# Kernel tuning notes

Hardware: AMD Instinct MI355X
Metric: run time of the kernel (lower is better)

## Reference

```python
import jax, jax.numpy as jnp
import numpy as np

# config (from UnifiedAttentionConfig defaults)
D = 512; H = 8; C = 64; DQ = 256; NI = 2; CI = 64
TOPK = 32; LMAX = 16; NWIN = 128; ROPE_BASE = 10000.0
B = 1; T = 1024; LP = 8; P = T // LP
NEG = -1e30


def _rope_cache(seq_len, dim):
    half = dim // 2
    inv = 1.0 / (ROPE_BASE ** (jnp.arange(half, dtype=jnp.float32) / half))
    f = jnp.arange(seq_len, dtype=jnp.float32)[:, None] * inv[None, :]
    emb = jnp.concatenate([f, f], axis=-1)
    return jnp.cos(emb), jnp.sin(emb)


def _rot(x, cos, sin):
    half = x.shape[-1] // 2
    x1, x2 = x[..., :half], x[..., half:]
    return x * cos + jnp.concatenate([-x2, x1], axis=-1) * sin


def _rms(x, w, eps=1e-6):
    return x * jax.lax.rsqrt(jnp.mean(x * x, axis=-1, keepdims=True) + eps) * w


def _forward(h, W_dq, W_uq, W_csa_kv, W_csa_z, B_csa, W_idx_kv, W_idx_z, B_idx,
             W_iuq, W_w, W_swkv, qnorm_w, knorm_w, W_o, sink_logits,
             phrase_mask, phrase_token_idx, phrase_end_pos):
    Bq, Tq, Dq = h.shape
    Pn, Lmax = phrase_mask.shape[1], phrase_mask.shape[2]
    scale = 1.0 / jnp.sqrt(jnp.float32(C))
    cos, sin = _rope_cache(Tq, C)
    cos_i, sin_i = _rope_cache(Tq, CI)
    # ---- queries: compress -> up-project -> RMSNorm -> RoPE (per-token) ----
    q_lat = h @ W_dq                                      # (B,T,DQ)
    q = (q_lat @ W_uq).reshape(Bq, Tq, H, C)
    q = _rot(_rms(q, qnorm_w), cos[:, None, :], sin[:, None, :])
    # ---- gather phrase tokens ----
    idx = phrase_token_idx.reshape(Bq, Pn * Lmax)
    hp = jnp.take_along_axis(h, idx[:, :, None], axis=1).reshape(Bq, Pn, Lmax, Dq)
    m = phrase_mask                                       # (B,P,Lmax) bool
    # ---- multi-head phrase compression (CSA KV) ----
    c_tok = (hp @ W_csa_kv).reshape(Bq, Pn, Lmax, H, C)
    z = (hp @ W_csa_z).reshape(Bq, Pn, Lmax, H, C) + B_csa[None, None]
    z = jnp.where(m[..., None, None], z, NEG)
    g = jax.nn.softmax(z, axis=2)
    g = jnp.where(m.any(axis=2)[:, :, None, None, None], g, 0.0)
    c_csa = jnp.sum(g * c_tok, axis=2)                    # (B,P,H,C) values
    pos = jnp.clip(phrase_end_pos, 0, Tq - 1)
    k_csa = _rot(_rms(c_csa, knorm_w), cos[pos][:, :, None, :], sin[pos][:, :, None, :])
    # ---- single-head phrase compression (indexer keys) ----
    ck = hp @ W_idx_kv                                    # (B,P,Lmax,CI)
    zk = hp @ W_idx_z + B_idx[None, None]
    zk = jnp.where(m[..., None], zk, NEG)
    gk = jax.nn.softmax(zk, axis=2)
    gk = jnp.where(m.any(axis=2)[:, :, None, None], gk, 0.0)
    k_idx = jnp.sum(gk * ck, axis=2)                      # (B,P,CI)
    k_idx = _rot(k_idx, cos_i[pos], sin_i[pos])
    # ---- lightning indexer + causal top-k routing ----
    q_i = (q_lat @ W_iuq).reshape(Bq, Tq, NI, CI)
    s = jax.nn.relu(jnp.einsum('bthd,bpd->bthp', q_i, k_idx))
    I = jnp.sum(s * (h @ W_w)[..., None], axis=2)         # (B,T,P)
    t_idx = jnp.arange(Tq)
    valid = (phrase_end_pos[:, None, :] <= t_idx[None, :, None]) & (phrase_end_pos[:, None, :] >= 0)
    I = jnp.where(valid, I, NEG)
    vals, sel = jax.lax.top_k(I, TOPK)                    # (B,T,K)
    sel_ok = vals > NEG * 0.5
    k_sel = jnp.take_along_axis(k_csa[:, None], sel[:, :, :, None, None], axis=2)  # (B,T,K,H,C)
    v_sel = jnp.take_along_axis(c_csa[:, None], sel[:, :, :, None, None], axis=2)
    logit_csa = jnp.einsum('bthc,btkhc->bthk', q, k_sel) * scale
    logit_csa = jnp.where(sel_ok[:, :, None, :], logit_csa, NEG)
    # ---- sliding window (fixed mode) ----
    kv = (h @ W_swkv).reshape(Bq, Tq, H, C)
    k_sw = _rot(_rms(kv, knorm_w), cos[:, None, :], sin[:, None, :])
    widx = t_idx[:, None] + jnp.arange(NWIN)[None, :] - (NWIN - 1)  # (T,W)
    w_ok = widx >= 0
    widx_c = jnp.clip(widx, 0, Tq - 1)
    k_win = k_sw[:, widx_c]                               # (B,T,W,H,C)
    v_win = kv[:, widx_c]
    logit_sw = jnp.einsum('bthc,btwhc->bthw', q, k_win) * scale
    logit_sw = jnp.where(w_ok[None, :, None, :], logit_sw, NEG)
    # ---- single softmax over [csa | window | sink] ----
    sink = jnp.broadcast_to(sink_logits.reshape(1, 1, H, 1), (Bq, Tq, H, 1))
    pattn = jax.nn.softmax(jnp.concatenate([logit_csa, logit_sw, sink], axis=-1), axis=-1)
    out = jnp.einsum('bthk,btkhc->bthc', pattn[..., :TOPK], v_sel) \
        + jnp.einsum('bthw,btwhc->bthc', pattn[..., TOPK:TOPK + NWIN], v_win)
    return out.reshape(Bq, Tq, H * C) @ W_o


def setup_inputs() -> dict:
    key = jax.random.key(0)
    ks = jax.random.split(key, 16)
    nrm = lambda k, shp: 0.02 * jax.random.normal(k, shp, dtype=jnp.float32)
    # structured phrases: phrase p covers tokens [p*LP, p*LP+LP), padded to LMAX
    l = np.arange(LMAX)
    mask = np.broadcast_to(l < LP, (B, P, LMAX)).copy()
    tok = np.minimum(l, LP - 1)[None, :] + (np.arange(P) * LP)[:, None]
    tok = np.broadcast_to(tok, (B, P, LMAX)).copy()
    end = np.broadcast_to(np.arange(P) * LP + LP - 1, (B, P)).copy()
    pid = np.broadcast_to(np.arange(T) // LP, (B, T)).copy()
    return {
        'h': jax.random.normal(ks[0], (B, T, D), dtype=jnp.float32),
        'phrase_mask': jnp.asarray(mask, dtype=bool),
        'phrase_token_idx': jnp.asarray(tok, dtype=jnp.int32),
        'phrase_end_pos': jnp.asarray(end, dtype=jnp.int32),
        'phrase_id': jnp.asarray(pid, dtype=jnp.int32),
        'W_dq': nrm(ks[1], (D, DQ)),
        'W_uq': nrm(ks[2], (DQ, H * C)),
        'W_csa_kv': nrm(ks[3], (D, H * C)),
        'W_csa_z': nrm(ks[4], (D, H * C)),
        'B_csa': nrm(ks[5], (LMAX, H, C)),
        'W_idx_kv': nrm(ks[6], (D, CI)),
        'W_idx_z': nrm(ks[7], (D, CI)),
        'B_idx': nrm(ks[8], (LMAX, CI)),
        'W_iuq': nrm(ks[9], (DQ, NI * CI)),
        'W_w': nrm(ks[10], (D, NI)),
        'W_swkv': nrm(ks[11], (D, H * C)),
        'qnorm_w': jnp.ones((C,), dtype=jnp.float32),
        'knorm_w': jnp.ones((C,), dtype=jnp.float32),
        'W_o': nrm(ks[12], (H * C, D)),
        'sink_logits': nrm(ks[13], (H,)),
    }


def reference(h, phrase_mask, phrase_token_idx, phrase_end_pos, phrase_id,
              W_dq, W_uq, W_csa_kv, W_csa_z, B_csa, W_idx_kv, W_idx_z, B_idx,
              W_iuq, W_w, W_swkv, qnorm_w, knorm_w, W_o, sink_logits):
    del phrase_id  # only used when sw_mode == 'phrase'
    return _forward(h, W_dq, W_uq, W_csa_kv, W_csa_z, B_csa, W_idx_kv, W_idx_z,
                    B_idx, W_iuq, W_w, W_swkv, qnorm_w, knorm_w, W_o, sink_logits,
                    phrase_mask, phrase_token_idx, phrase_end_pos)
```

## Files before the change

### kernel.cpp

```cpp
#include <hip/hip_runtime.h>
#include <cmath>

static constexpr int Tn = 1024, Dn = 512, Hn = 8, Cn = 64, DQn = 256,
                     NIn = 2, CIn = 64, TK = 32, LM = 16, NW = 128, Pn = 128;
#define NEGV (-1e30f)

typedef unsigned short u16;
typedef __bf16 bf16x8 __attribute__((ext_vector_type(8)));
typedef float f32x4 __attribute__((ext_vector_type(4)));

__device__ __forceinline__ u16 f2bf(float x) {
  unsigned u = __float_as_uint(x);
  return (u16)((u + 0x7fffu + ((u >> 16) & 1u)) >> 16);
}
__device__ __forceinline__ float bf2f(u16 b) {
  return __uint_as_float((unsigned)b << 16);
}

struct PackJobs {
  const float* src[7];
  u16* dst[7];
  int start[8];
  int N[7];
  int logN[7];
  int isA[7];
  int ps[7];
};

__global__ __launch_bounds__(256) void pack_all(PackJobs pj) {
  int i = blockIdx.x * 256 + threadIdx.x;
  if (i >= pj.start[7]) return;
  int j = 0;
  while (i >= pj.start[j + 1]) ++j;
  int local = i - pj.start[j];
  const float* s = pj.src[j];
  u16* dh = pj.dst[j];
  u16* dl = dh + pj.ps[j];
  float x[8];
  if (pj.isA[j]) {
    int kg = local & 63;
    int m = local >> 6;
    const float4* p = reinterpret_cast<const float4*>(s + (size_t)m * 512 + kg * 8);
    float4 a = p[0], b = p[1];
    x[0] = a.x; x[1] = a.y; x[2] = a.z; x[3] = a.w;
    x[4] = b.x; x[5] = b.y; x[6] = b.z; x[7] = b.w;
    union { u16 u[8]; int4 v; } oh, ol;
#pragma unroll
    for (int e = 0; e < 8; ++e) {
      u16 hb = f2bf(x[e]);
      oh.u[e] = hb;
      ol.u[e] = f2bf(x[e] - bf2f(hb));
    }
    size_t idx = ((size_t)kg * 1024 + m) * 8;
    *reinterpret_cast<int4*>(dh + idx) = oh.v;
    *reinterpret_cast<int4*>(dl + idx) = ol.v;
  } else {
    int N = pj.N[j];
    int n = local & (N - 1);
    int kg = local >> pj.logN[j];
#pragma unroll
    for (int e = 0; e < 8; ++e) x[e] = s[(size_t)(kg * 8 + e) * N + n];
    union { u16 u[8]; int4 v; } oh, ol;
#pragma unroll
    for (int e = 0; e < 8; ++e) {
      u16 hb = f2bf(x[e]);
      oh.u[e] = hb;
      ol.u[e] = f2bf(x[e] - bf2f(hb));
    }
    size_t idx = ((size_t)kg * N + n) * 8;
    *reinterpret_cast<int4*>(dh + idx) = oh.v;
    *reinterpret_cast<int4*>(dl + idx) = ol.v;
  }
}

struct TileDesc {
  const u16* Blo;
  const u16* Bhi;
  float* Clo;
  float* Chi;
  u16* Cp;
  int ldNlo, ldNhi, ldClo, ldChi, mode, n0, bps, cpps;
};
struct GemmArgs {
  TileDesc d[15];
};

#define GLD16(gp, lp)                                                     \
  __builtin_amdgcn_global_load_lds(                                      \
      (const __attribute__((address_space(1))) unsigned int*)(gp),       \
      (__attribute__((address_space(3))) unsigned int*)(lp), 16, 0, 0)

__global__ __launch_bounds__(256) void gemm_bf16(const u16* __restrict__ Ap,
                                                 int NK, int aps, GemmArgs ga) {
  const int ct = blockIdx.x, rt = blockIdx.y;
  const TileDesc d = ga.d[ct];
  const int m0 = rt * 128;
  __shared__ __align__(16) u16 lA[2][2][4][128][8];
  __shared__ __align__(16) u16 lB[2][2][4][128][8];
  const int tid = threadIdx.x;
  const int w = tid >> 6, lane = tid & 63;
  const int wm = w >> 1, wn = w & 1;

  f32x4 acc[4][4];
#pragma unroll
  for (int a = 0; a < 4; ++a)
#pragma unroll
    for (int b = 0; b < 4; ++b)
#pragma unroll
      for (int r = 0; r < 4; ++r) acc[a][b][r] = 0.f;

  auto stage = [&](int buf, int kg) {
    GLD16(Ap + ((size_t)kg * 1024 + m0 + lane) * 8, &lA[buf][0][w][0][0]);
    GLD16(Ap + ((size_t)kg * 1024 + m0 + 64 + lane) * 8, &lA[buf][0][w][64][0]);
    GLD16(Ap + aps + ((size_t)kg * 1024 + m0 + lane) * 8, &lA[buf][1][w][0][0]);
    GLD16(Ap + aps + ((size_t)kg * 1024 + m0 + 64 + lane) * 8, &lA[buf][1][w][64][0]);
    GLD16(d.Blo + ((size_t)kg * d.ldNlo + lane) * 8, &lB[buf][0][w][0][0]);
    GLD16(d.Bhi + ((size_t)kg * d.ldNhi + lane) * 8, &lB[buf][0][w][64][0]);
    GLD16(d.Blo + d.bps + ((size_t)kg * d.ldNlo + lane) * 8, &lB[buf][1][w][0][0]);
    GLD16(d.Bhi + d.bps + ((size_t)kg * d.ldNhi + lane) * 8, &lB[buf][1][w][64][0]);
  };

  stage(0, w);
  const int kq = lane >> 4, fr = lane & 15;
  for (int ks = 0; ks < NK; ++ks) {
    __syncthreads();
    if (ks + 1 < NK) stage((ks + 1) & 1, (ks + 1) * 4 + w);
    const int cb = ks & 1;
    bf16x8 aFh[4], aFl[4], bFh[4], bFl[4];
#pragma unroll
    for (int f = 0; f < 4; ++f) {
      aFh[f] = *reinterpret_cast<const bf16x8*>(&lA[cb][0][kq][wm * 64 + f * 16 + fr][0]);
      aFl[f] = *reinterpret_cast<const bf16x8*>(&lA[cb][1][kq][wm * 64 + f * 16 + fr][0]);
      bFh[f] = *reinterpret_cast<const bf16x8*>(&lB[cb][0][kq][wn * 64 + f * 16 + fr][0]);
      bFl[f] = *reinterpret_cast<const bf16x8*>(&lB[cb][1][kq][wn * 64 + f * 16 + fr][0]);
    }
#pragma unroll
    for (int fm = 0; fm < 4; ++fm)
#pragma unroll
      for (int fn = 0; fn < 4; ++fn) {
        acc[fm][fn] = __builtin_amdgcn_mfma_f32_16x16x32_bf16(aFh[fm], bFh[fn],
                                                              acc[fm][fn], 0, 0, 0);
        acc[fm][fn] = __builtin_amdgcn_mfma_f32_16x16x32_bf16(aFl[fm], bFh[fn],
                                                              acc[fm][fn], 0, 0, 0);
        acc[fm][fn] = __builtin_amdgcn_mfma_f32_16x16x32_bf16(aFh[fm], bFl[fn],
                                                              acc[fm][fn], 0, 0, 0);
      }
  }
  float* Cb = (wn == 0) ? d.Clo : d.Chi;
  const int ldc = (wn == 0) ? d.ldClo : d.ldChi;
  if (d.mode != 1) {
#pragma unroll
    for (int fm = 0; fm < 4; ++fm)
#pragma unroll
      for (int fn = 0; fn < 4; ++fn)
#pragma unroll
        for (int r = 0; r < 4; ++r) {
          int row = m0 + wm * 64 + fm * 16 + (lane >> 4) * 4 + r;
          int cl = fn * 16 + fr;
          Cb[(size_t)row * ldc + cl] = acc[fm][fn][r];
        }
  }
  if (d.mode >= 1) {
#pragma unroll
    for (int fm = 0; fm < 4; ++fm)
#pragma unroll
      for (int fn = 0; fn < 4; ++fn)
#pragma unroll
        for (int r = 0; r < 4; ++r) {
          int row = m0 + wm * 64 + fm * 16 + (lane >> 4) * 4 + r;
          int gc = d.n0 + wn * 64 + fn * 16 + fr;
          float v = acc[fm][fn][r];
          u16 hb = f2bf(v);
          u16 lb = f2bf(v - bf2f(hb));
          size_t idx = ((size_t)(gc >> 3) * 1024 + row) * 8 + (gc & 7);
          d.Cp[idx] = hb;
          d.Cp[idx + d.cpps] = lb;
        }
  }
}

__global__ __launch_bounds__(256) void idx_kernel(
    const float* __restrict__ h, const float* __restrict__ q_lat,
    const float* __restrict__ Wikv, const float* __restrict__ Wiz,
    const float* __restrict__ Wiuq, float* __restrict__ hikv,
    float* __restrict__ hiz, float* __restrict__ qib) {
  const int t = blockIdx.x;
  const int tid = threadIdx.x;
  __shared__ float hs[Dn];
  __shared__ float ql[DQn];
  hs[tid] = h[(size_t)t * Dn + tid];
  hs[tid + 256] = h[(size_t)t * Dn + tid + 256];
  ql[tid & 255] = q_lat[(size_t)t * DQn + (tid & 255)];
  __syncthreads();
  if (tid < 128) {
    const float* Wm = (tid < 64) ? Wikv : Wiz;
    const int ci = tid & 63;
    float a0 = 0.f, a1 = 0.f, a2 = 0.f, a3 = 0.f;
#pragma unroll 4
    for (int k = 0; k < Dn; k += 4) {
      a0 += hs[k + 0] * Wm[(k + 0) * CIn + ci];
      a1 += hs[k + 1] * Wm[(k + 1) * CIn + ci];
      a2 += hs[k + 2] * Wm[(k + 2) * CIn + ci];
      a3 += hs[k + 3] * Wm[(k + 3) * CIn + ci];
    }
    float acc = (a0 + a1) + (a2 + a3);
    if (tid < 64)
      hikv[(size_t)t * CIn + ci] = acc;
    else
      hiz[(size_t)t * CIn + ci] = acc;
  } else {
    const int jj = tid - 128;
    float a0 = 0.f, a1 = 0.f, a2 = 0.f, a3 = 0.f;
#pragma unroll 4
    for (int k = 0; k < DQn; k += 4) {
      a0 += ql[k + 0] * Wiuq[(k + 0) * 128 + jj];
      a1 += ql[k + 1] * Wiuq[(k + 1) * 128 + jj];
      a2 += ql[k + 2] * Wiuq[(k + 2) * 128 + jj];
      a3 += ql[k + 3] * Wiuq[(k + 3) * 128 + jj];
    }
    qib[(size_t)t * 128 + jj] = (a0 + a1) + (a2 + a3);
  }
}

__global__ __launch_bounds__(512) void phrase_kernel(
    const int* __restrict__ maskbuf, const int* __restrict__ tokbuf,
    const int* __restrict__ endbuf, const float* __restrict__ hckv,
    const float* __restrict__ hcz, const float* __restrict__ hikv,
    const float* __restrict__ hiz, const float* __restrict__ Bcsa,
    const float* __restrict__ Bidx, const float* __restrict__ knw,
    float* __restrict__ ccsa, float* __restrict__ kcsa,
    float* __restrict__ kidx) {
  const int p = blockIdx.x;
  const int tid = threadIdx.x;
  __shared__ int s_bytemode;
  __shared__ int s_tok[LM];
  __shared__ int s_m[LM];
  __shared__ int s_pos, s_anyv;

  if (tid == 0) s_bytemode = 0;
  __syncthreads();
  {
    unsigned w = ((const unsigned*)maskbuf)[tid];
    if (w > 1u) atomicOr(&s_bytemode, 1);
  }
  __syncthreads();
  const int bytemode = s_bytemode;
  if (tid < LM) {
    int mv;
    if (bytemode)
      mv = ((const unsigned char*)maskbuf)[p * LM + tid] != 0;
    else
      mv = maskbuf[p * LM + tid] != 0;
    s_m[tid] = mv;
    s_tok[tid] = tokbuf[p * LM + tid];
  }
  if (tid == 0) {
    int e = endbuf[p];
    s_pos = min(max(e, 0), Tn - 1);
  }
  __syncthreads();
  if (tid == 0) {
    int any = 0;
    for (int l = 0; l < LM; ++l) any |= s_m[l];
    s_anyv = any;
  }
  __syncthreads();
  const int anyv = s_anyv;
  const int pos = s_pos;
  const int c = tid & 63;
  const float fr = (float)pos * powf(10000.0f, -(float)(c & 31) / 32.0f);
  const float cv = cosf(fr), sv = sinf(fr);
  const float sgn = (c < 32) ? -1.f : 1.f;

  {
    float z[LM];
    float zmax = NEGV;
#pragma unroll
    for (int l = 0; l < LM; ++l) {
      float zv = hcz[s_tok[l] * Dn + tid] + Bcsa[l * (Hn * Cn) + tid];
      zv = s_m[l] ? zv : NEGV;
      z[l] = zv;
      zmax = fmaxf(zmax, zv);
    }
    float den = 0.f, num = 0.f;
#pragma unroll
    for (int l = 0; l < LM; ++l) {
      float e = expf(z[l] - zmax);
      den += e;
      num += e * hckv[s_tok[l] * Dn + tid];
    }
    float cc = anyv ? (num / den) : 0.f;
    ccsa[p * (Hn * Cn) + tid] = cc;

    float ss = cc * cc;
#pragma unroll
    for (int off = 32; off; off >>= 1) ss += __shfl_xor(ss, off, 64);
    float kn = cc * rsqrtf(ss / (float)Cn + 1e-6f) * knw[c];
    float pr = __shfl_xor(kn, 32, 64);
    kcsa[p * (Hn * Cn) + tid] = kn * cv + sgn * pr * sv;
  }

  if (tid < CIn) {
    float zk[LM];
    float zm = NEGV;
#pragma unroll
    for (int l = 0; l < LM; ++l) {
      float zv = hiz[s_tok[l] * CIn + tid] + Bidx[l * CIn + tid];
      zv = s_m[l] ? zv : NEGV;
      zk[l] = zv;
      zm = fmaxf(zm, zv);
    }
    float dk = 0.f, nk = 0.f;
#pragma unroll
    for (int l = 0; l < LM; ++l) {
      float e = expf(zk[l] - zm);
      dk += e;
      nk += e * hikv[s_tok[l] * CIn + tid];
    }
    float ki = anyv ? (nk / dk) : 0.f;
    float pr = __shfl_xor(ki, 32, 64);
    kidx[p * CIn + tid] = ki * cv + sgn * pr * sv;
  }
}

__global__ __launch_bounds__(512) void rmsrope_kernel(
    float* __restrict__ q, const float* __restrict__ kv,
    float* __restrict__ ksw, const float* __restrict__ qnw,
    const float* __restrict__ knw) {
  const int t = blockIdx.x;
  const int tid = threadIdx.x;
  const int c = tid & 63;
  const float fr = (float)t * powf(10000.0f, -(float)(c & 31) / 32.0f);
  const float cv = cosf(fr), sv = sinf(fr);
  const float sgn = (c < 32) ? -1.f : 1.f;
  {
    float x = q[t * Dn + tid];
    float ss = x * x;
#pragma unroll
    for (int off = 32; off; off >>= 1) ss += __shfl_xor(ss, off, 64);
    float xr = x * rsqrtf(ss / (float)Cn + 1e-6f) * qnw[c];
    float pr = __shfl_xor(xr, 32, 64);
    q[t * Dn + tid] = xr * cv + sgn * pr * sv;
  }
  {
    float y = kv[t * Dn + tid];
    float ss = y * y;
#pragma unroll
    for (int off = 32; off; off >>= 1) ss += __shfl_xor(ss, off, 64);
    float yr = y * rsqrtf(ss / (float)Cn + 1e-6f) * knw[c];
    float pr = __shfl_xor(yr, 32, 64);
    ksw[t * Dn + tid] = yr * cv + sgn * pr * sv;
  }
}

__global__ __launch_bounds__(128) void score_topk_kernel(
    const float* __restrict__ hbuf, const float* __restrict__ Ww,
    const float* __restrict__ qi, const float* __restrict__ kidx,
    const int* __restrict__ endbuf, int* __restrict__ sel,
    int* __restrict__ selok) {
  const int t = blockIdx.x;
  const int tid = threadIdx.x;
  __shared__ float sqi[NIn * CIn];
  __shared__ float sI[Pn];
  __shared__ float sp0[128], sp1[128];

  sqi[tid] = qi[t * (NIn * CIn) + tid];
  float p0 = 0.f, p1 = 0.f;
#pragma unroll
  for (int e4 = 0; e4 < 4; ++e4) {
    int e = tid * 4 + e4;
    float hv = hbuf[t * Dn + e];
    p0 += hv * Ww[e * NIn + 0];
    p1 += hv * Ww[e * NIn + 1];
  }
  sp0[tid] = p0;
  sp1[tid] = p1;
  __syncthreads();
  for (int srd = 64; srd; srd >>= 1) {
    if (tid < srd) {
      sp0[tid] += sp0[tid + srd];
      sp1[tid] += sp1[tid + srd];
    }
    __syncthreads();
  }
  const float ww0 = sp0[0], ww1 = sp1[0];

  {
    const int p = tid;
    const float* kp = &kidx[p * CIn];
    float s0 = 0.f, s1 = 0.f;
#pragma unroll 16
    for (int ci = 0; ci < CIn; ++ci) {
      float kc = kp[ci];
      s0 += sqi[ci] * kc;
      s1 += sqi[CIn + ci] * kc;
    }
    float Iv = fmaxf(s0, 0.f) * ww0 + fmaxf(s1, 0.f) * ww1;
    int e = endbuf[p];
    if (!(e <= t && e >= 0)) Iv = NEGV;
    sI[p] = Iv;
  }
  __syncthreads();

  if (tid < 64) {
    float v0 = sI[tid], v1 = sI[tid + 64];
    for (int it = 0; it < TK; ++it) {
      float bv;
      int bi;
      if (v0 >= v1) { bv = v0; bi = tid; } else { bv = v1; bi = tid + 64; }
#pragma unroll
      for (int off = 32; off; off >>= 1) {
        float ov = __shfl_xor(bv, off, 64);
        int oi = __shfl_xor(bi, off, 64);
        if (ov > bv || (ov == bv && oi < bi)) { bv = ov; bi = oi; }
      }
      if (tid == 0) {
        sel[t * TK + it] = bi;
        selok[t * TK + it] = (bv > NEGV * 0.5f) ? 1 : 0;
      }
      if (bi == tid) v0 = -3.4e38f;
      if (bi == tid + 64) v1 = -3.4e38f;
    }
  }
}

__global__ __launch_bounds__(256) void attn3_kernel(
    const float* __restrict__ q, const float* __restrict__ ksw,
    const float* __restrict__ kv, const float* __restrict__ kcsa,
    const float* __restrict__ ccsa, const int* __restrict__ sel,
    const int* __restrict__ selok, const float* __restrict__ sink,
    u16* __restrict__ atp) {
  const int tid = threadIdx.x;
  const int wid = tid >> 6, lane = tid & 63;
  const int g = lane >> 4;
  const int gl = lane & 15;
  const int pair = blockIdx.x * 4 + wid;
  const int t = pair >> 3, h = pair & 7;

  __shared__ float slog[4][164];
  __shared__ int s_sel[4][TK];
  __shared__ int s_ok[4][TK];

  if (lane < TK) {
    s_sel[wid][lane] = sel[t * TK + lane];
    s_ok[wid][lane] = selok[t * TK + lane];
  }
  const int hc = h * Cn + gl * 4;
  const float4 qf = *reinterpret_cast<const float4*>(&q[t * Dn + hc]);
  float* myslog = slog[wid];

#pragma unroll 4
  for (int pass = 0; pass < 32; ++pass) {
    int w = pass * 4 + g;
    int src = t + w - (NW - 1);
    int srcc = max(src, 0);
    float4 kk = *reinterpret_cast<const float4*>(&ksw[srcc * Dn + hc]);
    float acc = qf.x * kk.x + qf.y * kk.y + qf.z * kk.z + qf.w * kk.w;
#pragma unroll
    for (int off = 1; off < 16; off <<= 1) acc += __shfl_xor(acc, off, 64);
    if (gl == 0) myslog[TK + w] = (src >= 0) ? acc * 0.125f : NEGV;
  }
#pragma unroll 2
  for (int pass = 0; pass < 8; ++pass) {
    int s = pass * 4 + g;
    int se = s_sel[wid][s];
    float4 kk = *reinterpret_cast<const float4*>(&kcsa[se * Dn + hc]);
    float acc = qf.x * kk.x + qf.y * kk.y + qf.z * kk.z + qf.w * kk.w;
#pragma unroll
    for (int off = 1; off < 16; off <<= 1) acc += __shfl_xor(acc, off, 64);
    if (gl == 0) myslog[s] = s_ok[wid][s] ? acc * 0.125f : NEGV;
  }
  if (lane == 0) myslog[160] = sink[h];

  float x0 = myslog[lane];
  float x1 = myslog[lane + 64];
  float x2 = (lane < 33) ? myslog[lane + 128] : NEGV;
  float m = fmaxf(x0, fmaxf(x1, x2));
#pragma unroll
  for (int off = 32; off; off >>= 1) m = fmaxf(m, __shfl_xor(m, off, 64));
  float e0 = expf(x0 - m), e1 = expf(x1 - m);
  float e2 = (lane < 33) ? expf(x2 - m) : 0.f;
  float sden = e0 + e1 + e2;
#pragma unroll
  for (int off = 32; off; off >>= 1) sden += __shfl_xor(sden, off, 64);
  const float inv = 1.f / sden;
  myslog[lane] = e0 * inv;
  myslog[lane + 64] = e1 * inv;
  if (lane < 33) myslog[lane + 128] = e2 * inv;

  float4 acc = make_float4(0.f, 0.f, 0.f, 0.f);
#pragma unroll 4
  for (int pass = 0; pass < 32; ++pass) {
    int w = pass * 4 + g;
    int src = t + w - (NW - 1);
    int srcc = max(src, 0);
    float pv = myslog[TK + w];
    pv = (src >= 0) ? pv : 0.f;
    float4 vv = *reinterpret_cast<const float4*>(&kv[srcc * Dn + hc]);
    acc.x += pv * vv.x;
    acc.y += pv * vv.y;
    acc.z += pv * vv.z;
    acc.w += pv * vv.w;
  }
#pragma unroll 2
  for (int pass = 0; pass < 8; ++pass) {
    int s = pass * 4 + g;
    float pv = myslog[s];
    int se = s_sel[wid][s];
    float4 vv = *reinterpret_cast<const float4*>(&ccsa[se * Dn + hc]);
    acc.x += pv * vv.x;
    acc.y += pv * vv.y;
    acc.z += pv * vv.z;
    acc.w += pv * vv.w;
  }
  acc.x += __shfl_xor(acc.x, 16, 64);
  acc.y += __shfl_xor(acc.y, 16, 64);
  acc.z += __shfl_xor(acc.z, 16, 64);
  acc.w += __shfl_xor(acc.w, 16, 64);
  acc.x += __shfl_xor(acc.x, 32, 64);
  acc.y += __shfl_xor(acc.y, 32, 64);
  acc.z += __shfl_xor(acc.z, 32, 64);
  acc.w += __shfl_xor(acc.w, 32, 64);
  if (lane < 16) {
    float vals[4] = {acc.x, acc.y, acc.z, acc.w};
    int colb = h * Cn + lane * 4;
#pragma unroll
    for (int r = 0; r < 4; ++r) {
      int gc = colb + r;
      float v = vals[r];
      u16 hb = f2bf(v);
      u16 lb = f2bf(v - bf2f(hb));
      size_t idx = ((size_t)(gc >> 3) * 1024 + t) * 8 + (gc & 7);
      atp[idx] = hb;
      atp[idx + 524288] = lb;
    }
  }
}

extern "C" void kernel_launch(void* const* d_in, const int* in_sizes, int n_in,
                              void* d_out, int out_size, void* d_ws,
                              size_t ws_size, hipStream_t stream) {
  const float* h = (const float*)d_in[0];
  const int* mask = (const int*)d_in[1];
  const int* tok = (const int*)d_in[2];
  const int* endp = (const int*)d_in[3];
  const float* W_dq = (const float*)d_in[5];
  const float* W_uq = (const float*)d_in[6];
  const float* W_csa_kv = (const float*)d_in[7];
  const float* W_csa_z = (const float*)d_in[8];
  const float* B_csa = (const float*)d_in[9];
  const float* W_idx_kv = (const float*)d_in[10];
  const float* W_idx_z = (const float*)d_in[11];
  const float* B_idx = (const float*)d_in[12];
  const float* W_iuq = (const float*)d_in[13];
  const float* W_w = (const float*)d_in[14];
  const float* W_swkv = (const float*)d_in[15];
  const float* qnw = (const float*)d_in[16];
  const float* knw = (const float*)d_in[17];
  const float* W_o = (const float*)d_in[18];
  const float* sink = (const float*)d_in[19];

  float* ws = (float*)d_ws;
  u16* hA = (u16*)(ws + 0);
  float* qbuf = ws + 0;
  u16* qlP = (u16*)(ws + 524288);
  float* hckv = ws + 786432;
  u16* atP = (u16*)(ws + 786432);
  float* hcz = ws + 1310720;
  float* kswb = ws + 1310720;
  float* kvb = ws + 1835008;
  float* hikv = ws + 2359296;
  float* hiz = ws + 2424832;
  float* q_lat = ws + 2490368;
  float* ccsa = ws + 2752512;
  float* kcsa = ws + 2818048;
  float* kidx = ws + 2883584;
  int* seli = (int*)(ws + 2891776);
  int* selok = (int*)(ws + 2924544);
  u16* pW = (u16*)(ws + 2957312);
  u16* pWdq = pW;
  u16* pWckv = pWdq + 262144;
  u16* pWcz = pWckv + 524288;
  u16* pWsw = pWcz + 524288;
  u16* pWuq = pWsw + 524288;
  u16* pWo = pWuq + 262144;
  float* qib = ws + 4268032;
  float* outp = (float*)d_out;

  {
    PackJobs pj{};
    const float* srcs[7] = {h, W_dq, W_csa_kv, W_csa_z, W_swkv, W_uq, W_o};
    u16* dsts[7] = {hA, pWdq, pWckv, pWcz, pWsw, pWuq, pWo};
    int Ns[7] = {0, 256, 512, 512, 512, 512, 512};
    int logNs[7] = {0, 8, 9, 9, 9, 9, 9};
    int Ks[7] = {512, 512, 512, 512, 512, 256, 512};
    int isA[7] = {1, 0, 0, 0, 0, 0, 0};
    int pss[7] = {524288, 131072, 262144, 262144, 262144, 131072, 262144};
    int s = 0;
    for (int i = 0; i < 7; ++i) {
      pj.src[i] = srcs[i];
      pj.dst[i] = dsts[i];
      pj.N[i] = Ns[i];
      pj.logN[i] = logNs[i];
      pj.isA[i] = isA[i];
      pj.ps[i] = pss[i];
      pj.start[i] = s;
      s += isA[i] ? 1024 * (Ks[i] / 8) : (Ks[i] / 8) * Ns[i];
    }
    pj.start[7] = s;
    pack_all<<<(s + 255) / 256, 256, 0, stream>>>(pj);
  }

  auto normTile = [](const u16* pB, int N, int n0, float* C, int ldc, int bps) {
    TileDesc td{};
    td.Blo = pB + n0 * 8;
    td.Bhi = pB + (n0 + 64) * 8;
    td.ldNlo = td.ldNhi = N;
    td.Clo = C + n0;
    td.Chi = C + n0 + 64;
    td.ldClo = td.ldChi = ldc;
    td.mode = 0;
    td.bps = bps;
    return td;
  };

  {
    GemmArgs ga{};
    int nt = 0;
    for (int n0 = 0; n0 < 256; n0 += 128) {
      TileDesc td = normTile(pWdq, 256, n0, q_lat, 256, 131072);
      td.mode = 2;
      td.Cp = qlP;
      td.cpps = 262144;
      td.n0 = n0;
      ga.d[nt++] = td;
    }
    for (int n0 = 0; n0 < 512; n0 += 128) ga.d[nt++] = normTile(pWckv, 512, n0, hckv, 512, 262144);
    for (int n0 = 0; n0 < 512; n0 += 128) ga.d[nt++] = normTile(pWcz, 512, n0, hcz, 512, 262144);
    for (int n0 = 0; n0 < 512; n0 += 128) ga.d[nt++] = normTile(pWsw, 512, n0, kvb, 512, 262144);
    gemm_bf16<<<dim3(nt, 8), 256, 0, stream>>>(hA, 16, 524288, ga);
  }
  {
    GemmArgs ga{};
    int nt = 0;
    for (int n0 = 0; n0 < 512; n0 += 128) ga.d[nt++] = normTile(pWuq, 512, n0, qbuf, 512, 131072);
    gemm_bf16<<<dim3(nt, 8), 256, 0, stream>>>(qlP, 8, 262144, ga);
  }
  idx_kernel<<<Tn, 256, 0, stream>>>(h, q_lat, W_idx_kv, W_idx_z, W_iuq, hikv,
                                     hiz, qib);
  phrase_kernel<<<Pn, 512, 0, stream>>>(mask, tok, endp, hckv, hcz, hikv, hiz,
                                        B_csa, B_idx, knw, ccsa, kcsa, kidx);
  rmsrope_kernel<<<Tn, 512, 0, stream>>>(qbuf, kvb, kswb, qnw, knw);
  score_topk_kernel<<<Tn, 128, 0, stream>>>(h, W_w, qib, kidx, endp, seli,
                                            selok);
  attn3_kernel<<<dim3(Tn * Hn / 4), 256, 0, stream>>>(qbuf, kswb, kvb, kcsa,
                                                      ccsa, seli, selok, sink,
                                                      atP);
  {
    GemmArgs ga{};
    int nt = 0;
    for (int n0 = 0; n0 < 512; n0 += 128) ga.d[nt++] = normTile(pWo, 512, n0, outp, 512, 262144);
    gemm_bf16<<<dim3(nt, 8), 256, 0, stream>>>(atP, 16, 524288, ga);
  }
  (void)in_sizes; (void)n_in; (void)out_size; (void)ws_size;
}
```

Before: 154.5 us.

## Fuse phrase and RMS-RoPE kernels, batch idx tokens, transpose indexer keys in LDS

Merges the phrase compression kernel and the per-token RMSNorm+RoPE kernel into one launch whose extra blocks handle the token work, removing a launch and letting both run concurrently. The indexer projection kernel now processes four tokens per block, so each weight load is reused four times. The score kernel stages the indexer keys transposed in shared memory so per-phrase dot products read LDS instead of strided global memory. The h pack job's index mapping is changed so consecutive threads write consecutive output rows, and the workspace is relaid so ksw no longer aliases hcz, which the fused kernel reads in the same launch.

Result: faster. 151.1 us (-2.3%).

```diff
diff --git a/kernel.cpp b/kernel.cpp
--- a/kernel.cpp
+++ b/kernel.cpp
@@ -37,40 +37,32 @@
   u16* dh = pj.dst[j];
   u16* dl = dh + pj.ps[j];
   float x[8];
+  size_t idx;
   if (pj.isA[j]) {
-    int kg = local & 63;
-    int m = local >> 6;
+    int m = local & 1023;
+    int kg = local >> 10;
     const float4* p = reinterpret_cast<const float4*>(s + (size_t)m * 512 + kg * 8);
     float4 a = p[0], b = p[1];
     x[0] = a.x; x[1] = a.y; x[2] = a.z; x[3] = a.w;
     x[4] = b.x; x[5] = b.y; x[6] = b.z; x[7] = b.w;
-    union { u16 u[8]; int4 v; } oh, ol;
-#pragma unroll
-    for (int e = 0; e < 8; ++e) {
-      u16 hb = f2bf(x[e]);
-      oh.u[e] = hb;
-      ol.u[e] = f2bf(x[e] - bf2f(hb));
-    }
-    size_t idx = ((size_t)kg * 1024 + m) * 8;
-    *reinterpret_cast<int4*>(dh + idx) = oh.v;
-    *reinterpret_cast<int4*>(dl + idx) = ol.v;
+    idx = ((size_t)kg * 1024 + m) * 8;
   } else {
     int N = pj.N[j];
     int n = local & (N - 1);
     int kg = local >> pj.logN[j];
 #pragma unroll
     for (int e = 0; e < 8; ++e) x[e] = s[(size_t)(kg * 8 + e) * N + n];
-    union { u16 u[8]; int4 v; } oh, ol;
-#pragma unroll
-    for (int e = 0; e < 8; ++e) {
-      u16 hb = f2bf(x[e]);
-      oh.u[e] = hb;
-      ol.u[e] = f2bf(x[e] - bf2f(hb));
-    }
-    size_t idx = ((size_t)kg * N + n) * 8;
-    *reinterpret_cast<int4*>(dh + idx) = oh.v;
-    *reinterpret_cast<int4*>(dl + idx) = ol.v;
-  }
+    idx = ((size_t)kg * N + n) * 8;
+  }
+  union { u16 u[8]; int4 v; } oh, ol;
+#pragma unroll
+  for (int e = 0; e < 8; ++e) {
+    u16 hb = f2bf(x[e]);
+    oh.u[e] = hb;
+    ol.u[e] = f2bf(x[e] - bf2f(hb));
+  }
+  *reinterpret_cast<int4*>(dh + idx) = oh.v;
+  *reinterpret_cast<int4*>(dl + idx) = ol.v;
 }
 
 struct TileDesc {
@@ -184,54 +176,90 @@
     const float* __restrict__ Wikv, const float* __restrict__ Wiz,
     const float* __restrict__ Wiuq, float* __restrict__ hikv,
     float* __restrict__ hiz, float* __restrict__ qib) {
-  const int t = blockIdx.x;
+  const int t0 = blockIdx.x * 4;
   const int tid = threadIdx.x;
-  __shared__ float hs[Dn];
-  __shared__ float ql[DQn];
-  hs[tid] = h[(size_t)t * Dn + tid];
-  hs[tid + 256] = h[(size_t)t * Dn + tid + 256];
-  ql[tid & 255] = q_lat[(size_t)t * DQn + (tid & 255)];
+  __shared__ float hs[4][Dn];
+  __shared__ float ql[4][DQn];
+  for (int i = tid; i < 4 * Dn; i += 256)
+    hs[i >> 9][i & 511] = h[(size_t)(t0 + (i >> 9)) * Dn + (i & 511)];
+  for (int i = tid; i < 4 * DQn; i += 256)
+    ql[i >> 8][i & 255] = q_lat[(size_t)(t0 + (i >> 8)) * DQn + (i & 255)];
   __syncthreads();
   if (tid < 128) {
     const float* Wm = (tid < 64) ? Wikv : Wiz;
     const int ci = tid & 63;
     float a0 = 0.f, a1 = 0.f, a2 = 0.f, a3 = 0.f;
-#pragma unroll 4
-    for (int k = 0; k < Dn; k += 4) {
-      a0 += hs[k + 0] * Wm[(k + 0) * CIn + ci];
-      a1 += hs[k + 1] * Wm[(k + 1) * CIn + ci];
-      a2 += hs[k + 2] * Wm[(k + 2) * CIn + ci];
-      a3 += hs[k + 3] * Wm[(k + 3) * CIn + ci];
-    }
-    float acc = (a0 + a1) + (a2 + a3);
-    if (tid < 64)
-      hikv[(size_t)t * CIn + ci] = acc;
-    else
-      hiz[(size_t)t * CIn + ci] = acc;
+#pragma unroll 8
+    for (int k = 0; k < Dn; ++k) {
+      float wv = Wm[k * CIn + ci];
+      a0 += hs[0][k] * wv;
+      a1 += hs[1][k] * wv;
+      a2 += hs[2][k] * wv;
+      a3 += hs[3][k] * wv;
+    }
+    float* dst = (tid < 64) ? hikv : hiz;
+    dst[(size_t)(t0 + 0) * CIn + ci] = a0;
+    dst[(size_t)(t0 + 1) * CIn + ci] = a1;
+    dst[(size_t)(t0 + 2) * CIn + ci] = a2;
+    dst[(size_t)(t0 + 3) * CIn + ci] = a3;
   } else {
     const int jj = tid - 128;
     float a0 = 0.f, a1 = 0.f, a2 = 0.f, a3 = 0.f;
-#pragma unroll 4
-    for (int k = 0; k < DQn; k += 4) {
-      a0 += ql[k + 0] * Wiuq[(k + 0) * 128 + jj];
-      a1 += ql[k + 1] * Wiuq[(k + 1) * 128 + jj];
-      a2 += ql[k + 2] * Wiuq[(k + 2) * 128 + jj];
-      a3 += ql[k + 3] * Wiuq[(k + 3) * 128 + jj];
-    }
-    qib[(size_t)t * 128 + jj] = (a0 + a1) + (a2 + a3);
-  }
-}
-
-__global__ __launch_bounds__(512) void phrase_kernel(
+#pragma unroll 8
+    for (int k = 0; k < DQn; ++k) {
+      float wv = Wiuq[k * 128 + jj];
+      a0 += ql[0][k] * wv;
+      a1 += ql[1][k] * wv;
+      a2 += ql[2][k] * wv;
+      a3 += ql[3][k] * wv;
+    }
+    qib[(size_t)(t0 + 0) * 128 + jj] = a0;
+    qib[(size_t)(t0 + 1) * 128 + jj] = a1;
+    qib[(size_t)(t0 + 2) * 128 + jj] = a2;
+    qib[(size_t)(t0 + 3) * 128 + jj] = a3;
+  }
+}
+
+__global__ __launch_bounds__(512) void phrase_rope_kernel(
     const int* __restrict__ maskbuf, const int* __restrict__ tokbuf,
     const int* __restrict__ endbuf, const float* __restrict__ hckv,
     const float* __restrict__ hcz, const float* __restrict__ hikv,
     const float* __restrict__ hiz, const float* __restrict__ Bcsa,
     const float* __restrict__ Bidx, const float* __restrict__ knw,
-    float* __restrict__ ccsa, float* __restrict__ kcsa,
-    float* __restrict__ kidx) {
+    const float* __restrict__ qnw, float* __restrict__ ccsa,
+    float* __restrict__ kcsa, float* __restrict__ kidx,
+    float* __restrict__ q, const float* __restrict__ kv,
+    float* __restrict__ ksw) {
+  const int tid = threadIdx.x;
+  const int c = tid & 63;
+  const float sgn = (c < 32) ? -1.f : 1.f;
+
+  if (blockIdx.x >= Pn) {
+    const int t = blockIdx.x - Pn;
+    const float fr = (float)t * powf(10000.0f, -(float)(c & 31) / 32.0f);
+    const float cv = cosf(fr), sv = sinf(fr);
+    {
+      float x = q[t * Dn + tid];
+      float ss = x * x;
+#pragma unroll
+      for (int off = 32; off; off >>= 1) ss += __shfl_xor(ss, off, 64);
+      float xr = x * rsqrtf(ss / (float)Cn + 1e-6f) * qnw[c];
+      float pr = __shfl_xor(xr, 32, 64);
+      q[t * Dn + tid] = xr * cv + sgn * pr * sv;
+    }
+    {
+      float y = kv[t * Dn + tid];
+      float ss = y * y;
+#pragma unroll
+      for (int off = 32; off; off >>= 1) ss += __shfl_xor(ss, off, 64);
+      float yr = y * rsqrtf(ss / (float)Cn + 1e-6f) * knw[c];
+      float pr = __shfl_xor(yr, 32, 64);
+      ksw[t * Dn + tid] = yr * cv + sgn * pr * sv;
+    }
+    return;
+  }
+
   const int p = blockIdx.x;
-  const int tid = threadIdx.x;
   __shared__ int s_bytemode;
   __shared__ int s_tok[LM];
   __shared__ int s_m[LM];
@@ -240,8 +268,8 @@
   if (tid == 0) s_bytemode = 0;
   __syncthreads();
   {
-    unsigned w = ((const unsigned*)maskbuf)[tid];
-    if (w > 1u) atomicOr(&s_bytemode, 1);
+    unsigned wv = ((const unsigned*)maskbuf)[tid];
+    if (wv > 1u) atomicOr(&s_bytemode, 1);
   }
   __syncthreads();
   const int bytemode = s_bytemode;
@@ -267,10 +295,8 @@
   __syncthreads();
   const int anyv = s_anyv;
   const int pos = s_pos;
-  const int c = tid & 63;
   const float fr = (float)pos * powf(10000.0f, -(float)(c & 31) / 32.0f);
   const float cv = cosf(fr), sv = sinf(fr);
-  const float sgn = (c < 32) ? -1.f : 1.f;
 
   {
     float z[LM];
@@ -320,36 +346,6 @@
     float ki = anyv ? (nk / dk) : 0.f;
     float pr = __shfl_xor(ki, 32, 64);
     kidx[p * CIn + tid] = ki * cv + sgn * pr * sv;
-  }
-}
-
-__global__ __launch_bounds__(512) void rmsrope_kernel(
-    float* __restrict__ q, const float* __restrict__ kv,
-    float* __restrict__ ksw, const float* __restrict__ qnw,
-    const float* __restrict__ knw) {
-  const int t = blockIdx.x;
-  const int tid = threadIdx.x;
-  const int c = tid & 63;
-  const float fr = (float)t * powf(10000.0f, -(float)(c & 31) / 32.0f);
-  const float cv = cosf(fr), sv = sinf(fr);
-  const float sgn = (c < 32) ? -1.f : 1.f;
-  {
-    float x = q[t * Dn + tid];
-    float ss = x * x;
-#pragma unroll
-    for (int off = 32; off; off >>= 1) ss += __shfl_xor(ss, off, 64);
-    float xr = x * rsqrtf(ss / (float)Cn + 1e-6f) * qnw[c];
-    float pr = __shfl_xor(xr, 32, 64);
-    q[t * Dn + tid] = xr * cv + sgn * pr * sv;
-  }
-  {
-    float y = kv[t * Dn + tid];
-    float ss = y * y;
-#pragma unroll
-    for (int off = 32; off; off >>= 1) ss += __shfl_xor(ss, off, 64);
-    float yr = y * rsqrtf(ss / (float)Cn + 1e-6f) * knw[c];
-    float pr = __shfl_xor(yr, 32, 64);
-    ksw[t * Dn + tid] = yr * cv + sgn * pr * sv;
   }
 }
 
@@ -361,15 +357,27 @@
   const int t = blockIdx.x;
   const int tid = threadIdx.x;
   __shared__ float sqi[NIn * CIn];
+  __shared__ float kT[CIn][Pn + 1];
   __shared__ float sI[Pn];
   __shared__ float sp0[128], sp1[128];
 
-  sqi[tid] = qi[t * (NIn * CIn) + tid];
+  sqi[tid] = qi[(size_t)t * (NIn * CIn) + tid];
+#pragma unroll
+  for (int it = 0; it < 16; ++it) {
+    int idx4 = it * 128 + tid;
+    float4 v = reinterpret_cast<const float4*>(kidx)[idx4];
+    int p = idx4 >> 4;
+    int c4 = (idx4 & 15) * 4;
+    kT[c4 + 0][p] = v.x;
+    kT[c4 + 1][p] = v.y;
+    kT[c4 + 2][p] = v.z;
+    kT[c4 + 3][p] = v.w;
+  }
   float p0 = 0.f, p1 = 0.f;
 #pragma unroll
   for (int e4 = 0; e4 < 4; ++e4) {
     int e = tid * 4 + e4;
-    float hv = hbuf[t * Dn + e];
+    float hv = hbuf[(size_t)t * Dn + e];
     p0 += hv * Ww[e * NIn + 0];
     p1 += hv * Ww[e * NIn + 1];
   }
@@ -387,11 +395,10 @@
 
   {
     const int p = tid;
-    const float* kp = &kidx[p * CIn];
     float s0 = 0.f, s1 = 0.f;
 #pragma unroll 16
     for (int ci = 0; ci < CIn; ++ci) {
-      float kc = kp[ci];
+      float kc = kT[ci][p];
       s0 += sqi[ci] * kc;
       s1 += sqi[CIn + ci] * kc;
     }
@@ -567,7 +574,6 @@
   float* hckv = ws + 786432;
   u16* atP = (u16*)(ws + 786432);
   float* hcz = ws + 1310720;
-  float* kswb = ws + 1310720;
   float* kvb = ws + 1835008;
   float* hikv = ws + 2359296;
   float* hiz = ws + 2424832;
@@ -577,14 +583,15 @@
   float* kidx = ws + 2883584;
   int* seli = (int*)(ws + 2891776);
   int* selok = (int*)(ws + 2924544);
-  u16* pW = (u16*)(ws + 2957312);
+  float* qib = ws + 2957312;
+  float* kswb = ws + 3088384;
+  u16* pW = (u16*)(ws + 3612672);
   u16* pWdq = pW;
-  u16* pWckv = pWdq + 262144;
-  u16* pWcz = pWckv + 524288;
-  u16* pWsw = pWcz + 524288;
-  u16* pWuq = pWsw + 524288;
-  u16* pWo = pWuq + 262144;
-  float* qib = ws + 4268032;
+  u16* pWckv = pW + 262144;
+  u16* pWcz = pW + 786432;
+  u16* pWsw = pW + 1310720;
+  u16* pWuq = pW + 1835008;
+  u16* pWo = pW + 2097152;
   float* outp = (float*)d_out;
 
   {
@@ -646,11 +653,11 @@
     for (int n0 = 0; n0 < 512; n0 += 128) ga.d[nt++] = normTile(pWuq, 512, n0, qbuf, 512, 131072);
     gemm_bf16<<<dim3(nt, 8), 256, 0, stream>>>(qlP, 8, 262144, ga);
   }
-  idx_kernel<<<Tn, 256, 0, stream>>>(h, q_lat, W_idx_kv, W_idx_z, W_iuq, hikv,
-                                     hiz, qib);
-  phrase_kernel<<<Pn, 512, 0, stream>>>(mask, tok, endp, hckv, hcz, hikv, hiz,
-                                        B_csa, B_idx, knw, ccsa, kcsa, kidx);
-  rmsrope_kernel<<<Tn, 512, 0, stream>>>(qbuf, kvb, kswb, qnw, knw);
+  idx_kernel<<<Tn / 4, 256, 0, stream>>>(h, q_lat, W_idx_kv, W_idx_z, W_iuq,
+                                         hikv, hiz, qib);
+  phrase_rope_kernel<<<Pn + Tn, 512, 0, stream>>>(
+      mask, tok, endp, hckv, hcz, hikv, hiz, B_csa, B_idx, knw, qnw, ccsa,
+      kcsa, kidx, qbuf, kvb, kswb);
   score_topk_kernel<<<Tn, 128, 0, stream>>>(h, W_w, qib, kidx, endp, seli,
                                             selok);
   attn3_kernel<<<dim3(Tn * Hn / 4), 256, 0, stream>>>(qbuf, kswb, kvb, kcsa,
```
